# Kernel tuning notes

Measured on AMD Instinct MI355X. Metric: run time of the kernel, lower is better.

Reference implementation:

```python
import jax, jax.numpy as jnp
import numpy as np

B, T, D = 2, 2048, 1024
H = 16
HD = D // H  # head dim == config.k == config.v == 64


def setup_inputs() -> dict:
    key = jax.random.key(0)
    k1, k2, k3 = jax.random.split(key, 3)
    scale = 0.02
    x = jax.random.normal(k1, (B, T, D), dtype=jnp.float32)
    W1 = jax.random.normal(k2, (D, 3 * D), dtype=jnp.float32) * scale
    b1 = jnp.zeros((3 * D,), dtype=jnp.float32)
    W2 = jax.random.normal(k3, (D, D), dtype=jnp.float32) * scale
    b2 = jnp.zeros((D,), dtype=jnp.float32)
    return {"x": x, "W1": W1, "b1": b1, "W2": W2, "b2": b2}


def reference(x, W1, b1, W2, b2):
    # Fused QKV projection (dropout layers are identity in eval mode).
    Bx, Tx, C = x.shape
    qkv = x @ W1 + b1                      # [B, T, 3D]
    q, k, v = jnp.split(qkv, 3, axis=-1)   # each [B, T, D]
    q = q.reshape(Bx, Tx, H, HD).transpose(0, 2, 1, 3)  # [B, H, T, hd]
    k = k.reshape(Bx, Tx, H, HD).transpose(0, 2, 1, 3)
    v = v.reshape(Bx, Tx, H, HD).transpose(0, 2, 1, 3)

    logits = jnp.einsum('bhmk,bhnk->bhmn', q, k) / jnp.sqrt(jnp.float32(HD))
    # causal mask (lower-triangular bias buffer)
    causal = jnp.tril(jnp.ones((Tx, Tx), dtype=bool))
    logits = jnp.where(causal[None, None], logits, jnp.float32(-jnp.inf))
    att = jax.nn.softmax(logits, axis=-1)   # [B, H, T, T]

    y = jnp.einsum('bhmn,bhnv->bhmv', att, v)        # [B, H, T, hd]
    y = y.transpose(0, 2, 1, 3).reshape(Bx, Tx, C)   # [B, T, D]
    return y @ W2 + b2
```

## Files before the change

kernel.cpp:

```cpp
#include <hip/hip_runtime.h>

typedef __attribute__((ext_vector_type(8))) short bf16x8;
typedef __attribute__((ext_vector_type(4))) float f32x4;
typedef __attribute__((ext_vector_type(16))) float f32x16;
typedef __attribute__((ext_vector_type(4))) short short4v;
typedef __attribute__((ext_vector_type(4))) unsigned int uint4v;

#define B_  2
#define T_  2048
#define D_  1024
#define H_  16
#define HD_ 64

__device__ inline short f2bf(float f){
  unsigned u = __builtin_bit_cast(unsigned, f);
  u += 0x7fff + ((u >> 16) & 1);
  return (short)(u >> 16);
}

__device__ inline void gl2lds16(const void* g, void* l){
  __builtin_amdgcn_global_load_lds(
      (const __attribute__((address_space(1))) unsigned int*)g,
      (__attribute__((address_space(3))) unsigned int*)l, 16, 0, 0);
}

__device__ inline void transpose_tile(const float* __restrict__ in,
                                      short* __restrict__ out,
                                      int R, int C, int bx, int by){
  __shared__ float tile[32][33];
  int tx = threadIdx.x & 31, ty0 = threadIdx.x >> 5;
#pragma unroll
  for (int i = 0; i < 4; i++){
    int ty = ty0 + i * 8;
    tile[ty][tx] = in[(by + ty) * C + bx + tx];
  }
  __syncthreads();
#pragma unroll
  for (int i = 0; i < 4; i++){
    int ty = ty0 + i * 8;
    out[(bx + ty) * R + by + tx] = f2bf(tile[tx][ty]);
  }
}

__global__ __launch_bounds__(256) void prep(
    const float* __restrict__ x,  short* __restrict__ xb,
    const float* __restrict__ W1, short* __restrict__ W1T,
    const float* __restrict__ W2, short* __restrict__ W2T){
  const int bid = blockIdx.x;
  if (bid < 4096){
    int i = (bid * 256 + threadIdx.x) * 4;
    float4 v = *(const float4*)(x + i);
    short4v o;
    o[0] = f2bf(v.x); o[1] = f2bf(v.y); o[2] = f2bf(v.z); o[3] = f2bf(v.w);
    *(short4v*)(xb + i) = o;
  } else if (bid < 4096 + 3072){
    int tb = bid - 4096;
    transpose_tile(W1, W1T, 1024, 3072, (tb % 96) << 5, (tb / 96) << 5);
  } else {
    int tb = bid - 7168;
    transpose_tile(W2, W2T, 1024, 1024, (tb % 32) << 5, (tb / 32) << 5);
  }
}

#define BM 128
#define BN 128
#define BK 32

#define QSCALE 0.18033688011112042f

template<int N_, int K_, int EPI>
__global__ __launch_bounds__(256, 3) void gemm_bt(
    const short* __restrict__ A, const short* __restrict__ Bt,
    const float* __restrict__ bias,
    short* __restrict__ q, short* __restrict__ kk, short* __restrict__ vT,
    float* __restrict__ outf){
  __shared__ short As[3][BM * BK];
  __shared__ short Bs[3][BN * BK];
  const int tid = threadIdx.x;
  const int lane = tid & 63, w = tid >> 6;
  const int wm = w >> 1, wn = w & 1;
  const int lr = lane & 15, lk = lane >> 4;
  const int brow = blockIdx.y * BM, bcol = blockIdx.x * BN;
  f32x4 acc[4][4] = {};
  const short* Ag = A  + brow * K_;
  const short* Bg = Bt + bcol * K_;

  auto stage = [&](int buf, int k0){
#pragma unroll
    for (int i = 0; i < 2; i++){
      int idx = i * 256 + tid;
      int row = idx >> 2, c8 = (idx & 3) * 8;
      gl2lds16(Ag + row * K_ + k0 + c8, (char*)As[buf] + idx * 16);
      gl2lds16(Bg + row * K_ + k0 + c8, (char*)Bs[buf] + idx * 16);
    }
  };

  const int NT = K_ / BK;
  stage(0, 0);
  stage(1, BK);
  for (int t = 0; t < NT; ++t){
    if (t + 1 < NT)
      asm volatile("s_waitcnt vmcnt(4)" ::: "memory");
    else
      asm volatile("s_waitcnt vmcnt(0)" ::: "memory");
    __builtin_amdgcn_s_barrier();
    __builtin_amdgcn_sched_barrier(0);
    if (t + 2 < NT)
      stage((t + 2) % 3, (t + 2) * BK);
    __builtin_amdgcn_sched_barrier(0);

    const short* Ac = As[t % 3];
    const short* Bc = Bs[t % 3];
    bf16x8 a[4], b[4];
#pragma unroll
    for (int mf = 0; mf < 4; mf++)
      a[mf] = *(const bf16x8*)(Ac + (wm * 64 + mf * 16 + lr) * BK + lk * 8);
#pragma unroll
    for (int nf = 0; nf < 4; nf++)
      b[nf] = *(const bf16x8*)(Bc + (wn * 64 + nf * 16 + lr) * BK + lk * 8);
    __builtin_amdgcn_s_setprio(1);
#pragma unroll
    for (int mf = 0; mf < 4; mf++)
#pragma unroll
      for (int nf = 0; nf < 4; nf++)
        acc[mf][nf] = __builtin_amdgcn_mfma_f32_16x16x32_bf16(a[mf], b[nf], acc[mf][nf], 0, 0, 0);
    __builtin_amdgcn_s_setprio(0);
  }

  if constexpr (EPI == 0){
#pragma unroll
    for (int nf = 0; nf < 4; nf++){
      int n = bcol + wn * 64 + nf * 16 + lr;
      float bv = bias[n];
      int sec = n >> 10, d = n & 1023, h = d >> 6, hd = d & 63;
#pragma unroll
      for (int mf = 0; mf < 4; mf++){
        int m0 = brow + wm * 64 + mf * 16 + lk * 4;
        int b = m0 >> 11, t0 = m0 & 2047;
        int bh = b * H_ + h;
        if (sec == 0){
#pragma unroll
          for (int r = 0; r < 4; r++)
            q[(bh * T_ + t0 + r) * HD_ + hd] = f2bf((acc[mf][nf][r] + bv) * QSCALE);
        } else if (sec == 1){
#pragma unroll
          for (int r = 0; r < 4; r++)
            kk[(bh * T_ + t0 + r) * HD_ + hd] = f2bf(acc[mf][nf][r] + bv);
        } else {
          float v0 = acc[mf][nf][0] + bv, v1 = acc[mf][nf][1] + bv;
          float v2 = acc[mf][nf][2] + bv, v3 = acc[mf][nf][3] + bv;
          unsigned lo = (unsigned)(unsigned short)f2bf(v0) | ((unsigned)(unsigned short)f2bf(v1) << 16);
          unsigned hi = (unsigned)(unsigned short)f2bf(v2) | ((unsigned)(unsigned short)f2bf(v3) << 16);
          uint2 pk; pk.x = lo; pk.y = hi;
          *(uint2*)(vT + (bh * HD_ + hd) * T_ + t0) = pk;
        }
      }
    }
  } else {
#pragma unroll
    for (int nf = 0; nf < 4; nf++){
      int n = bcol + wn * 64 + nf * 16 + lr;
      float bv = bias[n];
#pragma unroll
      for (int mf = 0; mf < 4; mf++){
        int m0 = brow + wm * 64 + mf * 16 + lk * 4;
#pragma unroll
        for (int r = 0; r < 4; r++)
          outf[(m0 + r) * N_ + n] = acc[mf][nf][r] + bv;
      }
    }
  }
}

__device__ inline int crow(int r, int h){ return (r & 3) + 8 * (r >> 2) + 4 * h; }

template<int SPLIT>
__global__ __launch_bounds__(256, 4) void attn32(
    const short* __restrict__ Q, const short* __restrict__ Kg,
    const short* __restrict__ Vt, short* __restrict__ Y,
    float* __restrict__ Op, float* __restrict__ ml){
  __shared__ short Ks[2][64 * 64];
  __shared__ short Vs[2][64 * 64];
  __shared__ float bounce[4][32];
  const int tid = threadIdx.x;
  const int w = tid >> 6, l = tid & 63;
  const int lq = l & 31, h = l >> 5;
  const int bx = blockIdx.x;
  int i, hf;
  if constexpr (SPLIT){
    int u = bx >> 5, v = u & 15;
    i = (v < 8) ? 15 - v : v - 8;
    hf = u >> 4;
  } else {
    i = (bx < 256) ? 15 - (bx >> 5) : (bx >> 5) - 8;
    hf = 0;
  }
  const int bh = bx & 31;
  const int q0 = i * 128, qw = q0 + w * 32;
  const int t0 = (SPLIT && hf) ? (i + 1) : 0;
  const int t1 = (SPLIT && !hf) ? (i + 1) : 2 * (i + 1);

  bf16x8 qb[4];
  {
    const short* qbase = Q + (bh * T_ + qw + lq) * HD_;
#pragma unroll
    for (int dk = 0; dk < 4; dk++)
      qb[dk] = *(const bf16x8*)(qbase + dk * 16 + h * 8);
  }

  f32x16 o0 = {}, o1 = {};
  float m = -1e30f, ll = 0.f;

  auto stage = [&](int buf, int t){
#pragma unroll
    for (int j = 0; j < 2; j++){
      int idx = j * 256 + tid;
      int row = idx >> 3, cb = (idx & 7) * 16;
      int cbs = cb ^ ((row & 7) << 4);
      gl2lds16(Kg + (bh * T_ + t * 64 + row) * HD_ + (cbs >> 1), (char*)Ks[buf] + idx * 16);
      gl2lds16(Vt + (bh * HD_ + row) * T_ + t * 64 + (cbs >> 1), (char*)Vs[buf] + idx * 16);
    }
  };

  stage(0, t0);
  for (int t = t0; t < t1; ++t){
    const int cur = (t - t0) & 1;
    if (t + 1 < t1){
      stage(cur ^ 1, t + 1);
      asm volatile("s_waitcnt vmcnt(4)" ::: "memory");
    } else {
      asm volatile("s_waitcnt vmcnt(0)" ::: "memory");
    }
    __builtin_amdgcn_s_barrier();
    __builtin_amdgcn_sched_barrier(0);

    const int kvb = t * 64;
    if (kvb <= qw + 31){
      const short* Kc = Ks[cur];
      const short* Vc = Vs[cur];

      f32x16 s[2] = {};
      __builtin_amdgcn_s_setprio(1);
#pragma unroll
      for (int kb = 0; kb < 2; kb++){
        int row = kb * 32 + lq;
        const char* rp = (const char*)Kc + row * 128;
        int swz = (row & 7) << 4;
#pragma unroll
        for (int dk = 0; dk < 4; dk++){
          bf16x8 ka = *(const bf16x8*)(rp + ((dk * 32 + h * 16) ^ swz));
          s[kb] = __builtin_amdgcn_mfma_f32_32x32x16_bf16(ka, qb[dk], s[kb], 0, 0, 0);
        }
      }
      __builtin_amdgcn_s_setprio(0);

      const int qg = qw + lq;
      if (kvb + 63 > qw){
#pragma unroll
        for (int kb = 0; kb < 2; kb++)
#pragma unroll
          for (int r = 0; r < 16; r++){
            int kv = kvb + kb * 32 + crow(r, h);
            if (kv > qg) s[kb][r] = -1e30f;
          }
      }

      float pm = s[0][0];
#pragma unroll
      for (int r = 1; r < 16; r++) pm = fmaxf(pm, s[0][r]);
#pragma unroll
      for (int r = 0; r < 16; r++) pm = fmaxf(pm, s[1][r]);
      pm = fmaxf(pm, __shfl_xor(pm, 32));

      if (__any(pm > m + 8.f)){
        float mn = fmaxf(pm, m);
        float sf = __builtin_amdgcn_exp2f(m - mn);
        m = mn;
        ll *= sf;
        bounce[w][lq] = sf;
#pragma unroll
        for (int r = 0; r < 16; r++){
          float sr = bounce[w][crow(r, h)];
          o0[r] *= sr; o1[r] *= sr;
        }
      }

      float ts = 0.f;
#pragma unroll
      for (int kb = 0; kb < 2; kb++)
#pragma unroll
        for (int r = 0; r < 16; r++){
          float p = __builtin_amdgcn_exp2f(s[kb][r] - m);
          s[kb][r] = p;
          ts += p;
        }
      ts += __shfl_xor(ts, 32);
      ll += ts;

      unsigned pw0[8], pw1[8];
#pragma unroll
      for (int kb = 0; kb < 2; kb++)
#pragma unroll
        for (int gg = 0; gg < 4; gg++){
          unsigned r0, r1;
          asm("v_cvt_pk_bf16_f32 %0, %1, %2" : "=v"(r0) : "v"(s[kb][gg * 4 + 0]), "v"(s[kb][gg * 4 + 1]));
          asm("v_cvt_pk_bf16_f32 %0, %1, %2" : "=v"(r1) : "v"(s[kb][gg * 4 + 2]), "v"(s[kb][gg * 4 + 3]));
          pw0[kb * 4 + gg] = r0;
          pw1[kb * 4 + gg] = r1;
        }
#pragma unroll
      for (int ks = 0; ks < 4; ks++){
        asm("v_permlane32_swap_b32 %0, %1" : "+v"(pw0[2 * ks]), "+v"(pw0[2 * ks + 1]));
        asm("v_permlane32_swap_b32 %0, %1" : "+v"(pw1[2 * ks]), "+v"(pw1[2 * ks + 1]));
      }

      __builtin_amdgcn_s_setprio(1);
#pragma unroll
      for (int ks = 0; ks < 4; ks++){
        uint4v paw;
        paw[0] = pw0[2 * ks];     paw[1] = pw1[2 * ks];
        paw[2] = pw0[2 * ks + 1]; paw[3] = pw1[2 * ks + 1];
        bf16x8 pa = __builtin_bit_cast(bf16x8, paw);
#pragma unroll
        for (int nb = 0; nb < 2; nb++){
          int row = nb * 32 + lq;
          bf16x8 vb = *(const bf16x8*)((const char*)Vc + row * 128 +
                        ((ks * 32 + h * 16) ^ ((row & 7) << 4)));
          if (nb == 0) o0 = __builtin_amdgcn_mfma_f32_32x32x16_bf16(pa, vb, o0, 0, 0, 0);
          else         o1 = __builtin_amdgcn_mfma_f32_32x32x16_bf16(pa, vb, o1, 0, 0, 0);
        }
      }
      __builtin_amdgcn_s_setprio(0);
    }
    __builtin_amdgcn_sched_barrier(0);
    __builtin_amdgcn_s_barrier();
  }

  if constexpr (SPLIT){
    float* Oq = Op + ((size_t)(hf * 32 + bh)) * (size_t)T_ * 64;
    if (h == 0){
      float* mlr = ml + ((size_t)(hf * 32 + bh) * T_ + (qw + lq)) * 2;
      mlr[0] = m; mlr[1] = ll;
    }
#pragma unroll
    for (int r = 0; r < 16; r++){
      int qg = qw + crow(r, h);
      Oq[qg * 64 + lq]      = o0[r];
      Oq[qg * 64 + 32 + lq] = o1[r];
    }
  } else {
    bounce[w][lq] = __builtin_amdgcn_rcpf(ll);
    const int b = bh >> 4, hh = bh & 15;
#pragma unroll
    for (int r = 0; r < 16; r++){
      int row = crow(r, h);
      float rl = bounce[w][row];
      int qg = qw + row;
      short* yb = Y + (b * T_ + qg) * D_ + hh * 64;
      yb[lq]      = f2bf(o0[r] * rl);
      yb[32 + lq] = f2bf(o1[r] * rl);
    }
  }
}

__global__ __launch_bounds__(256) void attn_merge(
    const float* __restrict__ Op, const float* __restrict__ ml,
    short* __restrict__ Y){
  int gid = blockIdx.x * 256 + threadIdx.x;
  int rid = gid >> 2, c16 = (gid & 3) * 16;
  float m1 = ml[rid * 2],           l1 = ml[rid * 2 + 1];
  float m2 = ml[131072 + rid * 2],  l2 = ml[131072 + rid * 2 + 1];
  float M  = fmaxf(m1, m2);
  float f1 = __builtin_amdgcn_exp2f(m1 - M);
  float f2 = __builtin_amdgcn_exp2f(m2 - M);
  float rl = 1.f / (f1 * l1 + f2 * l2);
  f1 *= rl; f2 *= rl;
  const float4* O1 = (const float4*)(Op + (size_t)rid * 64 + c16);
  const float4* O2 = (const float4*)(Op + 4194304ull + (size_t)rid * 64 + c16);
  int bh = rid >> 11, t = rid & 2047;
  short* yb = Y + (((bh >> 4) * T_ + t) * D_) + (bh & 15) * 64 + c16;
#pragma unroll
  for (int j = 0; j < 4; j++){
    float4 a = O1[j], b = O2[j];
    short4v o;
    o[0] = f2bf(f1 * a.x + f2 * b.x);
    o[1] = f2bf(f1 * a.y + f2 * b.y);
    o[2] = f2bf(f1 * a.z + f2 * b.z);
    o[3] = f2bf(f1 * a.w + f2 * b.w);
    *(short4v*)(yb + j * 4) = o;
  }
}

extern "C" void kernel_launch(void* const* d_in, const int* in_sizes, int n_in,
                              void* d_out, int out_size, void* d_ws, size_t ws_size,
                              hipStream_t stream) {
  const float* x  = (const float*)d_in[0];
  const float* W1 = (const float*)d_in[1];
  const float* b1 = (const float*)d_in[2];
  const float* W2 = (const float*)d_in[3];
  const float* b2 = (const float*)d_in[4];
  float* out = (float*)d_out;

  char* ws = (char*)d_ws;
  short* W1T = (short*)(ws);
  short* W2T = (short*)(ws + 6291456);
  short* xb  = (short*)(ws + 8388608);
  short* q   = (short*)(ws + 16777216);
  short* kk  = (short*)(ws + 25165824);
  short* vT  = (short*)(ws + 33554432);
  float* Op  = (float*)(ws + 41943040);
  float* mlb = (float*)(ws + 41943040 + 33554432);
  short* y   = xb;

  const size_t need = 41943040ull + 33554432ull + 1048576ull;
  const bool split = ws_size >= need;

  prep<<<dim3(8192), dim3(256), 0, stream>>>(x, xb, W1, W1T, W2, W2T);
  gemm_bt<3072, 1024, 0><<<dim3(24, 32), dim3(256), 0, stream>>>(xb, W1T, b1, q, kk, vT, nullptr);
  if (split){
    attn32<1><<<dim3(1024), dim3(256), 0, stream>>>(q, kk, vT, nullptr, Op, mlb);
    attn_merge<<<dim3(1024), dim3(256), 0, stream>>>(Op, mlb, y);
  } else {
    attn32<0><<<dim3(512), dim3(256), 0, stream>>>(q, kk, vT, y, nullptr, nullptr);
  }
  gemm_bt<1024, 1024, 1><<<dim3(8, 32), dim3(256), 0, stream>>>(y, W2T, b2, nullptr, nullptr, nullptr, out);
}
```

Measured before the change: 116.2 us.

## Split attention KV range four ways and store partial outputs in bf16

Generalises the split-KV attention from two halves to NS partitions, launching four times as many blocks for the causal attention than the unsplit path. The goal is better CU occupancy and load balance across the triangular workload. Partial outputs are now stored as bf16 instead of fp32, which halves the partial-output traffic into the merge kernel. The merge kernel now combines four partials with vectorised loads. The row max and sum buffer is moved into the no-longer-needed W1T workspace region. In exchange, K/V staging and Q loads are repeated per split, and bf16 rounding of the unnormalised partials costs some precision.

Result: faster. 111.5 us (-4.1%).

```diff
diff --git a/kernel.cpp b/kernel.cpp
--- a/kernel.cpp
+++ b/kernel.cpp
@@ -16,6 +16,10 @@
   unsigned u = __builtin_bit_cast(unsigned, f);
   u += 0x7fff + ((u >> 16) & 1);
   return (short)(u >> 16);
+}
+__device__ inline float bf2f(short s){
+  unsigned u = ((unsigned)(unsigned short)s) << 16;
+  return __builtin_bit_cast(float, u);
 }
 
 __device__ inline void gl2lds16(const void* g, void* l){
@@ -174,11 +178,11 @@
 
 __device__ inline int crow(int r, int h){ return (r & 3) + 8 * (r >> 2) + 4 * h; }
 
-template<int SPLIT>
+template<int NS>
 __global__ __launch_bounds__(256, 4) void attn32(
     const short* __restrict__ Q, const short* __restrict__ Kg,
     const short* __restrict__ Vt, short* __restrict__ Y,
-    float* __restrict__ Op, float* __restrict__ ml){
+    short* __restrict__ Op, float* __restrict__ ml){
   __shared__ short Ks[2][64 * 64];
   __shared__ short Vs[2][64 * 64];
   __shared__ float bounce[4][32];
@@ -187,7 +191,7 @@
   const int lq = l & 31, h = l >> 5;
   const int bx = blockIdx.x;
   int i, hf;
-  if constexpr (SPLIT){
+  if constexpr (NS == 4){
     int u = bx >> 5, v = u & 15;
     i = (v < 8) ? 15 - v : v - 8;
     hf = u >> 4;
@@ -197,8 +201,9 @@
   }
   const int bh = bx & 31;
   const int q0 = i * 128, qw = q0 + w * 32;
-  const int t0 = (SPLIT && hf) ? (i + 1) : 0;
-  const int t1 = (SPLIT && !hf) ? (i + 1) : 2 * (i + 1);
+  const int nt = 2 * (i + 1);
+  const int t0 = hf * nt / NS;
+  const int t1 = (hf + 1) * nt / NS;
 
   bf16x8 qb[4];
   {
@@ -222,122 +227,124 @@
     }
   };
 
-  stage(0, t0);
-  for (int t = t0; t < t1; ++t){
-    const int cur = (t - t0) & 1;
-    if (t + 1 < t1){
-      stage(cur ^ 1, t + 1);
-      asm volatile("s_waitcnt vmcnt(4)" ::: "memory");
-    } else {
-      asm volatile("s_waitcnt vmcnt(0)" ::: "memory");
-    }
-    __builtin_amdgcn_s_barrier();
-    __builtin_amdgcn_sched_barrier(0);
-
-    const int kvb = t * 64;
-    if (kvb <= qw + 31){
-      const short* Kc = Ks[cur];
-      const short* Vc = Vs[cur];
-
-      f32x16 s[2] = {};
-      __builtin_amdgcn_s_setprio(1);
-#pragma unroll
-      for (int kb = 0; kb < 2; kb++){
-        int row = kb * 32 + lq;
-        const char* rp = (const char*)Kc + row * 128;
-        int swz = (row & 7) << 4;
-#pragma unroll
-        for (int dk = 0; dk < 4; dk++){
-          bf16x8 ka = *(const bf16x8*)(rp + ((dk * 32 + h * 16) ^ swz));
-          s[kb] = __builtin_amdgcn_mfma_f32_32x32x16_bf16(ka, qb[dk], s[kb], 0, 0, 0);
-        }
+  if (t0 < t1){
+    stage(0, t0);
+    for (int t = t0; t < t1; ++t){
+      const int cur = (t - t0) & 1;
+      if (t + 1 < t1){
+        stage(cur ^ 1, t + 1);
+        asm volatile("s_waitcnt vmcnt(4)" ::: "memory");
+      } else {
+        asm volatile("s_waitcnt vmcnt(0)" ::: "memory");
       }
-      __builtin_amdgcn_s_setprio(0);
-
-      const int qg = qw + lq;
-      if (kvb + 63 > qw){
+      __builtin_amdgcn_s_barrier();
+      __builtin_amdgcn_sched_barrier(0);
+
+      const int kvb = t * 64;
+      if (kvb <= qw + 31){
+        const short* Kc = Ks[cur];
+        const short* Vc = Vs[cur];
+
+        f32x16 s[2] = {};
+        __builtin_amdgcn_s_setprio(1);
+#pragma unroll
+        for (int kb = 0; kb < 2; kb++){
+          int row = kb * 32 + lq;
+          const char* rp = (const char*)Kc + row * 128;
+          int swz = (row & 7) << 4;
+#pragma unroll
+          for (int dk = 0; dk < 4; dk++){
+            bf16x8 ka = *(const bf16x8*)(rp + ((dk * 32 + h * 16) ^ swz));
+            s[kb] = __builtin_amdgcn_mfma_f32_32x32x16_bf16(ka, qb[dk], s[kb], 0, 0, 0);
+          }
+        }
+        __builtin_amdgcn_s_setprio(0);
+
+        const int qg = qw + lq;
+        if (kvb + 63 > qw){
+#pragma unroll
+          for (int kb = 0; kb < 2; kb++)
+#pragma unroll
+            for (int r = 0; r < 16; r++){
+              int kv = kvb + kb * 32 + crow(r, h);
+              if (kv > qg) s[kb][r] = -1e30f;
+            }
+        }
+
+        float pm = s[0][0];
+#pragma unroll
+        for (int r = 1; r < 16; r++) pm = fmaxf(pm, s[0][r]);
+#pragma unroll
+        for (int r = 0; r < 16; r++) pm = fmaxf(pm, s[1][r]);
+        pm = fmaxf(pm, __shfl_xor(pm, 32));
+
+        if (__any(pm > m + 8.f)){
+          float mn = fmaxf(pm, m);
+          float sf = __builtin_amdgcn_exp2f(m - mn);
+          m = mn;
+          ll *= sf;
+          bounce[w][lq] = sf;
+#pragma unroll
+          for (int r = 0; r < 16; r++){
+            float sr = bounce[w][crow(r, h)];
+            o0[r] *= sr; o1[r] *= sr;
+          }
+        }
+
+        float ts = 0.f;
 #pragma unroll
         for (int kb = 0; kb < 2; kb++)
 #pragma unroll
           for (int r = 0; r < 16; r++){
-            int kv = kvb + kb * 32 + crow(r, h);
-            if (kv > qg) s[kb][r] = -1e30f;
+            float p = __builtin_amdgcn_exp2f(s[kb][r] - m);
+            s[kb][r] = p;
+            ts += p;
           }
+        ts += __shfl_xor(ts, 32);
+        ll += ts;
+
+        unsigned pw0[8], pw1[8];
+#pragma unroll
+        for (int kb = 0; kb < 2; kb++)
+#pragma unroll
+          for (int gg = 0; gg < 4; gg++){
+            unsigned r0, r1;
+            asm("v_cvt_pk_bf16_f32 %0, %1, %2" : "=v"(r0) : "v"(s[kb][gg * 4 + 0]), "v"(s[kb][gg * 4 + 1]));
+            asm("v_cvt_pk_bf16_f32 %0, %1, %2" : "=v"(r1) : "v"(s[kb][gg * 4 + 2]), "v"(s[kb][gg * 4 + 3]));
+            pw0[kb * 4 + gg] = r0;
+            pw1[kb * 4 + gg] = r1;
+          }
+#pragma unroll
+        for (int ks = 0; ks < 4; ks++){
+          asm("v_permlane32_swap_b32 %0, %1" : "+v"(pw0[2 * ks]), "+v"(pw0[2 * ks + 1]));
+          asm("v_permlane32_swap_b32 %0, %1" : "+v"(pw1[2 * ks]), "+v"(pw1[2 * ks + 1]));
+        }
+
+        __builtin_amdgcn_s_setprio(1);
+#pragma unroll
+        for (int ks = 0; ks < 4; ks++){
+          uint4v paw;
+          paw[0] = pw0[2 * ks];     paw[1] = pw1[2 * ks];
+          paw[2] = pw0[2 * ks + 1]; paw[3] = pw1[2 * ks + 1];
+          bf16x8 pa = __builtin_bit_cast(bf16x8, paw);
+#pragma unroll
+          for (int nb = 0; nb < 2; nb++){
+            int row = nb * 32 + lq;
+            bf16x8 vb = *(const bf16x8*)((const char*)Vc + row * 128 +
+                          ((ks * 32 + h * 16) ^ ((row & 7) << 4)));
+            if (nb == 0) o0 = __builtin_amdgcn_mfma_f32_32x32x16_bf16(pa, vb, o0, 0, 0, 0);
+            else         o1 = __builtin_amdgcn_mfma_f32_32x32x16_bf16(pa, vb, o1, 0, 0, 0);
+          }
+        }
+        __builtin_amdgcn_s_setprio(0);
       }
-
-      float pm = s[0][0];
-#pragma unroll
-      for (int r = 1; r < 16; r++) pm = fmaxf(pm, s[0][r]);
-#pragma unroll
-      for (int r = 0; r < 16; r++) pm = fmaxf(pm, s[1][r]);
-      pm = fmaxf(pm, __shfl_xor(pm, 32));
-
-      if (__any(pm > m + 8.f)){
-        float mn = fmaxf(pm, m);
-        float sf = __builtin_amdgcn_exp2f(m - mn);
-        m = mn;
-        ll *= sf;
-        bounce[w][lq] = sf;
-#pragma unroll
-        for (int r = 0; r < 16; r++){
-          float sr = bounce[w][crow(r, h)];
-          o0[r] *= sr; o1[r] *= sr;
-        }
-      }
-
-      float ts = 0.f;
-#pragma unroll
-      for (int kb = 0; kb < 2; kb++)
-#pragma unroll
-        for (int r = 0; r < 16; r++){
-          float p = __builtin_amdgcn_exp2f(s[kb][r] - m);
-          s[kb][r] = p;
-          ts += p;
-        }
-      ts += __shfl_xor(ts, 32);
-      ll += ts;
-
-      unsigned pw0[8], pw1[8];
-#pragma unroll
-      for (int kb = 0; kb < 2; kb++)
-#pragma unroll
-        for (int gg = 0; gg < 4; gg++){
-          unsigned r0, r1;
-          asm("v_cvt_pk_bf16_f32 %0, %1, %2" : "=v"(r0) : "v"(s[kb][gg * 4 + 0]), "v"(s[kb][gg * 4 + 1]));
-          asm("v_cvt_pk_bf16_f32 %0, %1, %2" : "=v"(r1) : "v"(s[kb][gg * 4 + 2]), "v"(s[kb][gg * 4 + 3]));
-          pw0[kb * 4 + gg] = r0;
-          pw1[kb * 4 + gg] = r1;
-        }
-#pragma unroll
-      for (int ks = 0; ks < 4; ks++){
-        asm("v_permlane32_swap_b32 %0, %1" : "+v"(pw0[2 * ks]), "+v"(pw0[2 * ks + 1]));
-        asm("v_permlane32_swap_b32 %0, %1" : "+v"(pw1[2 * ks]), "+v"(pw1[2 * ks + 1]));
-      }
-
-      __builtin_amdgcn_s_setprio(1);
-#pragma unroll
-      for (int ks = 0; ks < 4; ks++){
-        uint4v paw;
-        paw[0] = pw0[2 * ks];     paw[1] = pw1[2 * ks];
-        paw[2] = pw0[2 * ks + 1]; paw[3] = pw1[2 * ks + 1];
-        bf16x8 pa = __builtin_bit_cast(bf16x8, paw);
-#pragma unroll
-        for (int nb = 0; nb < 2; nb++){
-          int row = nb * 32 + lq;
-          bf16x8 vb = *(const bf16x8*)((const char*)Vc + row * 128 +
-                        ((ks * 32 + h * 16) ^ ((row & 7) << 4)));
-          if (nb == 0) o0 = __builtin_amdgcn_mfma_f32_32x32x16_bf16(pa, vb, o0, 0, 0, 0);
-          else         o1 = __builtin_amdgcn_mfma_f32_32x32x16_bf16(pa, vb, o1, 0, 0, 0);
-        }
-      }
-      __builtin_amdgcn_s_setprio(0);
-    }
-    __builtin_amdgcn_sched_barrier(0);
-    __builtin_amdgcn_s_barrier();
-  }
-
-  if constexpr (SPLIT){
-    float* Oq = Op + ((size_t)(hf * 32 + bh)) * (size_t)T_ * 64;
+      __builtin_amdgcn_sched_barrier(0);
+      __builtin_amdgcn_s_barrier();
+    }
+  }
+
+  if constexpr (NS == 4){
+    short* Oq = Op + ((size_t)(hf * 32 + bh)) * (size_t)T_ * 64;
     if (h == 0){
       float* mlr = ml + ((size_t)(hf * 32 + bh) * T_ + (qw + lq)) * 2;
       mlr[0] = m; mlr[1] = ll;
@@ -345,8 +352,8 @@
 #pragma unroll
     for (int r = 0; r < 16; r++){
       int qg = qw + crow(r, h);
-      Oq[qg * 64 + lq]      = o0[r];
-      Oq[qg * 64 + 32 + lq] = o1[r];
+      Oq[qg * 64 + lq]      = f2bf(o0[r]);
+      Oq[qg * 64 + 32 + lq] = f2bf(o1[r]);
     }
   } else {
     bounce[w][lq] = __builtin_amdgcn_rcpf(ll);
@@ -364,31 +371,47 @@
 }
 
 __global__ __launch_bounds__(256) void attn_merge(
-    const float* __restrict__ Op, const float* __restrict__ ml,
+    const short* __restrict__ Op, const float* __restrict__ ml,
     short* __restrict__ Y){
   int gid = blockIdx.x * 256 + threadIdx.x;
   int rid = gid >> 2, c16 = (gid & 3) * 16;
-  float m1 = ml[rid * 2],           l1 = ml[rid * 2 + 1];
-  float m2 = ml[131072 + rid * 2],  l2 = ml[131072 + rid * 2 + 1];
-  float M  = fmaxf(m1, m2);
-  float f1 = __builtin_amdgcn_exp2f(m1 - M);
-  float f2 = __builtin_amdgcn_exp2f(m2 - M);
-  float rl = 1.f / (f1 * l1 + f2 * l2);
-  f1 *= rl; f2 *= rl;
-  const float4* O1 = (const float4*)(Op + (size_t)rid * 64 + c16);
-  const float4* O2 = (const float4*)(Op + 4194304ull + (size_t)rid * 64 + c16);
+  float mh[4], lh[4];
+#pragma unroll
+  for (int hf = 0; hf < 4; hf++){
+    float2 v = *(const float2*)(ml + (size_t)hf * 131072 + rid * 2);
+    mh[hf] = v.x; lh[hf] = v.y;
+  }
+  float M = fmaxf(fmaxf(mh[0], mh[1]), fmaxf(mh[2], mh[3]));
+  float f[4], den = 0.f;
+#pragma unroll
+  for (int hf = 0; hf < 4; hf++){
+    f[hf] = __builtin_amdgcn_exp2f(mh[hf] - M);
+    den += f[hf] * lh[hf];
+  }
+  float rl = 1.f / den;
+  float acc[16] = {};
+#pragma unroll
+  for (int hf = 0; hf < 4; hf++){
+    const short* o = Op + (size_t)hf * 4194304 + (size_t)rid * 64 + c16;
+    bf16x8 a = *(const bf16x8*)(o);
+    bf16x8 b = *(const bf16x8*)(o + 8);
+    float fh = f[hf];
+#pragma unroll
+    for (int j = 0; j < 8; j++){
+      acc[j]     += fh * bf2f(a[j]);
+      acc[8 + j] += fh * bf2f(b[j]);
+    }
+  }
   int bh = rid >> 11, t = rid & 2047;
   short* yb = Y + (((bh >> 4) * T_ + t) * D_) + (bh & 15) * 64 + c16;
-#pragma unroll
-  for (int j = 0; j < 4; j++){
-    float4 a = O1[j], b = O2[j];
-    short4v o;
-    o[0] = f2bf(f1 * a.x + f2 * b.x);
-    o[1] = f2bf(f1 * a.y + f2 * b.y);
-    o[2] = f2bf(f1 * a.z + f2 * b.z);
-    o[3] = f2bf(f1 * a.w + f2 * b.w);
-    *(short4v*)(yb + j * 4) = o;
-  }
+  bf16x8 o0, o1;
+#pragma unroll
+  for (int j = 0; j < 8; j++){
+    o0[j] = f2bf(acc[j] * rl);
+    o1[j] = f2bf(acc[8 + j] * rl);
+  }
+  *(bf16x8*)(yb)     = o0;
+  *(bf16x8*)(yb + 8) = o1;
 }
 
 extern "C" void kernel_launch(void* const* d_in, const int* in_sizes, int n_in,
@@ -408,20 +431,20 @@
   short* q   = (short*)(ws + 16777216);
   short* kk  = (short*)(ws + 25165824);
   short* vT  = (short*)(ws + 33554432);
-  float* Op  = (float*)(ws + 41943040);
-  float* mlb = (float*)(ws + 41943040 + 33554432);
+  short* Op  = (short*)(ws + 41943040);
+  float* mlb = (float*)(ws);
   short* y   = xb;
 
-  const size_t need = 41943040ull + 33554432ull + 1048576ull;
+  const size_t need = 41943040ull + 33554432ull;
   const bool split = ws_size >= need;
 
   prep<<<dim3(8192), dim3(256), 0, stream>>>(x, xb, W1, W1T, W2, W2T);
   gemm_bt<3072, 1024, 0><<<dim3(24, 32), dim3(256), 0, stream>>>(xb, W1T, b1, q, kk, vT, nullptr);
   if (split){
-    attn32<1><<<dim3(1024), dim3(256), 0, stream>>>(q, kk, vT, nullptr, Op, mlb);
+    attn32<4><<<dim3(2048), dim3(256), 0, stream>>>(q, kk, vT, nullptr, Op, mlb);
     attn_merge<<<dim3(1024), dim3(256), 0, stream>>>(Op, mlb, y);
   } else {
-    attn32<0><<<dim3(512), dim3(256), 0, stream>>>(q, kk, vT, y, nullptr, nullptr);
+    attn32<1><<<dim3(512), dim3(256), 0, stream>>>(q, kk, vT, y, nullptr, nullptr);
   }
   gemm_bt<1024, 1024, 1><<<dim3(8, 32), dim3(256), 0, stream>>>(y, W2T, b2, nullptr, nullptr, nullptr, out);
 }
```
